# Kernel tuning notes

Hardware: AMD Instinct MI355X
Metric: run time of the kernel (lower is better)

## Reference

```python
import jax, jax.numpy as jnp
import numpy as np

B, C, H, W = 16, 64, 64, 64
HEADS = 8

def conv1x1(x, w):
    # x: [B, Cin, H, W], w: [Cout, Cin] -> [B, Cout, H, W]
    return jnp.einsum('oc,bchw->bohw', w, x)

def maxpool2x2(x):
    b, c, h, w = x.shape
    return x.reshape(b, c, h // 2, 2, w // 2, 2).max(axis=(3, 5))

def setup_inputs() -> dict:
    key = jax.random.key(0)
    ks = jax.random.split(key, 6)
    x = jax.random.normal(ks[0], (B, C, H, W), dtype=jnp.float32)
    w_theta = jax.random.normal(ks[1], (C // HEADS, C), dtype=jnp.float32) * 0.05
    w_phi = jax.random.normal(ks[2], (C // HEADS, C), dtype=jnp.float32) * 0.05
    w_g = jax.random.normal(ks[3], (C // 2, C), dtype=jnp.float32) * 0.05
    w_o = jax.random.normal(ks[4], (C, C // 2), dtype=jnp.float32) * 0.05
    gamma = jax.random.normal(ks[5], (), dtype=jnp.float32)
    return {'x': x, 'w_theta': w_theta, 'w_phi': w_phi, 'w_g': w_g, 'w_o': w_o, 'gamma': gamma}

def reference(x, w_theta, w_phi, w_g, w_o, gamma):
    b, c, h, w = x.shape
    n = h * w                      # query length
    m = n // 4                     # kv length after 2x2 maxpool
    theta = conv1x1(x, w_theta).reshape(b, c // HEADS, n)   # [B, C/h, N]
    phi = maxpool2x2(conv1x1(x, w_phi)).reshape(b, c // HEADS, m)  # [B, C/h, M]
    g = maxpool2x2(conv1x1(x, w_g)).reshape(b, c // 2, m)   # [B, C/2, M]
    # attention: theta^T @ phi -> [B, N, M]; NOTE: no 1/sqrt(d) scaling (SAGAN)
    beta = jax.nn.softmax(jnp.einsum('bdn,bdm->bnm', theta, phi), axis=-1)
    # o = g @ beta^T -> [B, C/2, N]
    o = jnp.einsum('bdm,bnm->bdn', g, beta).reshape(b, c // 2, h, w)
    o = conv1x1(o, w_o)            # [B, C, H, W]
    return gamma * o + x
```

## Files before the change

kernel.cpp:

```cpp
#include <hip/hip_runtime.h>
#include <hip/hip_bf16.h>

#define NB 16
#define NC 64
#define NN 4096
#define NM 1024
#define ND 8
#define NG 32

typedef short short8 __attribute__((ext_vector_type(8)));
typedef float floatx4 __attribute__((ext_vector_type(4)));

#define LOG2E 1.44269504f

__device__ __forceinline__ short f2bfs(float f) {
    union { __hip_bfloat16 h; short s; } u;
    u.h = __float2bfloat16(f);
    return u.s;
}
__device__ __forceinline__ unsigned pack2bf(float a, float b) {
    return (unsigned)(unsigned short)f2bfs(a) | ((unsigned)(unsigned short)f2bfs(b) << 16);
}
__device__ __forceinline__ unsigned pk2fast(float a, float b) {
    unsigned ua = __float_as_uint(a) + 0x8000u;
    unsigned ub = __float_as_uint(b) + 0x8000u;
    return __builtin_amdgcn_perm(ub, ua, 0x07060302);
}
__device__ __forceinline__ short8 u4s8(uint4 v) {
    union { uint4 u; short8 s; } c; c.u = v; return c.s;
}

__global__ __launch_bounds__(256)
void proj_kernel(const float* __restrict__ x,
                 const float* __restrict__ w_phi,
                 const float* __restrict__ w_g,
                 const float* __restrict__ w_o,
                 unsigned* __restrict__ phi_ws,
                 unsigned* __restrict__ g2_ws)
{
    __shared__ __align__(16) float xl[64 * 128];
    __shared__ float lwpT[64 * 8];
    __shared__ __align__(8) float lwgT[64 * 34];
    __shared__ float lwoT[32 * 65];
    __shared__ __align__(16) float lgs[32 * 36];
    __shared__ float lps[32 * 8];

    const int b  = blockIdx.x >> 5;
    const int ph = blockIdx.x & 31;
    const int t  = threadIdx.x;

    for (int i = t; i < 512; i += 256) lwpT[(i & 63) * 8 + (i >> 6)] = w_phi[i];
    for (int i = t; i < 2048; i += 256) {
        lwgT[(i & 63) * 34 + (i >> 6)] = w_g[i];
        lwoT[(i & 31) * 65 + (i >> 5)] = w_o[i];
    }

    const float* xb = x + (size_t)b * NC * NN + (size_t)ph * 128;
    for (int idx = t; idx < 2048; idx += 256) {
        int c = idx >> 5, i4 = idx & 31;
        ((float4*)xl)[c * 32 + i4] = ((const float4*)(xb + (size_t)c * NN))[i4];
    }
    __syncthreads();

    {
        int oc = t >> 3, grp = t & 7;
        float s0[16];
        #pragma unroll
        for (int i = 0; i < 16; ++i) s0[i] = 0.f;
        const float4* xl4 = (const float4*)xl;
        #pragma unroll 4
        for (int c = 0; c < 64; ++c) {
            float4 a0 = xl4[c * 32 + 2 * grp];
            float4 a1 = xl4[c * 32 + 2 * grp + 1];
            float4 b0 = xl4[c * 32 + 16 + 2 * grp];
            float4 b1 = xl4[c * 32 + 17 + 2 * grp];
            float w0 = lwgT[c * 34 + oc];
            s0[0] = fmaf(w0, a0.x, s0[0]);  s0[1] = fmaf(w0, a0.y, s0[1]);
            s0[2] = fmaf(w0, a0.z, s0[2]);  s0[3] = fmaf(w0, a0.w, s0[3]);
            s0[4] = fmaf(w0, a1.x, s0[4]);  s0[5] = fmaf(w0, a1.y, s0[5]);
            s0[6] = fmaf(w0, a1.z, s0[6]);  s0[7] = fmaf(w0, a1.w, s0[7]);
            s0[8] = fmaf(w0, b0.x, s0[8]);  s0[9] = fmaf(w0, b0.y, s0[9]);
            s0[10] = fmaf(w0, b0.z, s0[10]); s0[11] = fmaf(w0, b0.w, s0[11]);
            s0[12] = fmaf(w0, b1.x, s0[12]); s0[13] = fmaf(w0, b1.y, s0[13]);
            s0[14] = fmaf(w0, b1.z, s0[14]); s0[15] = fmaf(w0, b1.w, s0[15]);
        }
        #pragma unroll
        for (int p = 0; p < 4; ++p)
            lgs[oc * 36 + grp * 4 + p] =
                fmaxf(fmaxf(s0[2 * p], s0[2 * p + 1]), fmaxf(s0[8 + 2 * p], s0[9 + 2 * p]));
    }

    {
        int m = t >> 3, oc = t & 7;
        float s0 = 0.f, s1 = 0.f, s2 = 0.f, s3 = 0.f;
        #pragma unroll 4
        for (int c = 0; c < 64; ++c) {
            float w = lwpT[c * 8 + oc];
            const float* xr = &xl[c * 128];
            s0 = fmaf(w, xr[2 * m],      s0);
            s1 = fmaf(w, xr[2 * m + 1],  s1);
            s2 = fmaf(w, xr[64 + 2 * m], s2);
            s3 = fmaf(w, xr[65 + 2 * m], s3);
        }
        lps[m * 8 + oc] = fmaxf(fmaxf(s0, s1), fmaxf(s2, s3));
    }
    __syncthreads();

    {
        int co = t >> 2, sel = t & 3;
        int m0a = 4 * sel, m0b = 16 + 4 * sel;
        float v[8];
        #pragma unroll
        for (int mm = 0; mm < 8; ++mm) v[mm] = 0.f;
        #pragma unroll 4
        for (int c = 0; c < 32; ++c) {
            float w = lwoT[c * 65 + co];
            float4 ga = *(const float4*)&lgs[c * 36 + m0a];
            float4 gb = *(const float4*)&lgs[c * 36 + m0b];
            v[0] = fmaf(w, ga.x, v[0]); v[1] = fmaf(w, ga.y, v[1]);
            v[2] = fmaf(w, ga.z, v[2]); v[3] = fmaf(w, ga.w, v[3]);
            v[4] = fmaf(w, gb.x, v[4]); v[5] = fmaf(w, gb.y, v[5]);
            v[6] = fmaf(w, gb.z, v[6]); v[7] = fmaf(w, gb.w, v[7]);
        }
        uint4 pk;
        pk.x = pack2bf(v[0], v[1]); pk.y = pack2bf(v[2], v[3]);
        pk.z = pack2bf(v[4], v[5]); pk.w = pack2bf(v[6], v[7]);
        int lane = (sel << 4) | (co & 15);
        ((uint4*)g2_ws)[(((size_t)b * 4 + (co >> 4)) * 32 + ph) * 64 + lane] = pk;
    }

    if (t < 32) {
        const float* pr = &lps[t * 8];
        uint4 pk;
        pk.x = pack2bf(pr[0], pr[1]); pk.y = pack2bf(pr[2], pr[3]);
        pk.z = pack2bf(pr[4], pr[5]); pk.w = pack2bf(pr[6], pr[7]);
        ((uint4*)phi_ws)[(size_t)b * NM + ph * 32 + t] = pk;
    }
}

#define KG_STEP(CPP0, CPP1, CG)                                                          \
    {                                                                                    \
        _Pragma("unroll")                                                                \
        for (int qt = 0; qt < 2; ++qt) {                                                 \
            floatx4 s0 = __builtin_amdgcn_mfma_f32_16x16x32_bf16(                        \
                u4s8(CPP0), u4s8(tb[qt]), (floatx4)0.f, 0, 0, 0);                        \
            floatx4 s1 = __builtin_amdgcn_mfma_f32_16x16x32_bf16(                        \
                u4s8(CPP1), u4s8(tb[qt]), (floatx4)0.f, 0, 0, 0);                        \
            float e0[4], e1[4];                                                          \
            _Pragma("unroll")                                                            \
            for (int r = 0; r < 4; ++r) {                                                \
                e0[r] = __builtin_amdgcn_exp2f(s0[r]);                                   \
                e1[r] = __builtin_amdgcn_exp2f(s1[r]);                                   \
            }                                                                            \
            lsum[qt] += ((e0[0] + e0[1]) + (e0[2] + e0[3]))                              \
                      + ((e1[0] + e1[1]) + (e1[2] + e1[3]));                             \
            uint4 pb = make_uint4(pk2fast(e0[0], e0[1]), pk2fast(e0[2], e0[3]),          \
                                  pk2fast(e1[0], e1[1]), pk2fast(e1[2], e1[3]));         \
            _Pragma("unroll")                                                            \
            for (int ct = 0; ct < 4; ++ct)                                               \
                acc[qt][ct] = __builtin_amdgcn_mfma_f32_16x16x32_bf16(                   \
                    u4s8(CG[ct]), u4s8(pb), acc[qt][ct], 0, 0, 0);                       \
        }                                                                                \
    }

__global__ __launch_bounds__(256, 2)
void attn_kernel(const unsigned* __restrict__ phi_ws,
                 const unsigned* __restrict__ g2_ws,
                 const float* __restrict__ w_theta,
                 const float* __restrict__ gamma_p,
                 const float* __restrict__ x,
                 float* __restrict__ out)
{
    __shared__ __align__(16) float smem[14080];
    uint4* lphi = (uint4*)smem;
    float* lwt  = smem + 4096;
    float* lth  = smem + 4608;
    float* lx   = smem + 5632;
    float* ltr  = smem + 4608;

    const int b    = blockIdx.x >> 5;
    const int qblk = blockIdx.x & 31;
    const int t    = threadIdx.x;
    const int w    = t >> 6;
    const int lane = t & 63;
    const int lm   = lane & 15;
    const int quad = lane >> 4;
    const int q0   = qblk * 128 + w * 32;

    const uint4* gf = (const uint4*)g2_ws;
    uint4 gA[4], gB[4];
    #pragma unroll
    for (int ct = 0; ct < 4; ++ct) {
        gA[ct] = gf[(((size_t)b * 4 + ct) * 32 + 0) * 64 + lane];
        gB[ct] = gf[(((size_t)b * 4 + ct) * 32 + 1) * 64 + lane];
    }

    for (int kk = t; kk < NM; kk += 256)
        lphi[kk] = ((const uint4*)phi_ws)[(size_t)b * NM + kk];
    for (int i = t; i < 512; i += 256) lwt[i] = w_theta[i];
    {
        const float* xb = x + (size_t)b * NC * NN + (size_t)qblk * 128;
        for (int idx = t; idx < 2048; idx += 256) {
            int c = idx >> 5, i4 = idx & 31;
            ((float4*)(lx + c * 132))[i4] = ((const float4*)(xb + (size_t)c * NN))[i4];
        }
    }
    __syncthreads();

    {
        int qi = t & 127, och = (t >> 7) * 4;
        float th4[4] = {0.f, 0.f, 0.f, 0.f};
        for (int c = 0; c < 64; ++c) {
            float xv = lx[c * 132 + qi];
            #pragma unroll
            for (int o = 0; o < 4; ++o)
                th4[o] = fmaf(lwt[(och + o) * 64 + c], xv, th4[o]);
        }
        *(float4*)&lth[qi * 8 + och] = make_float4(th4[0], th4[1], th4[2], th4[3]);
    }
    __syncthreads();

    uint4 tb[2];
    #pragma unroll
    for (int qt = 0; qt < 2; ++qt) {
        const float* thp = &lth[(w * 32 + qt * 16 + lm) * 8];
        float4 a = ((const float4*)thp)[0], c4 = ((const float4*)thp)[1];
        uint4 v;
        v.x = pack2bf(a.x * LOG2E, a.y * LOG2E);
        v.y = pack2bf(a.z * LOG2E, a.w * LOG2E);
        v.z = pack2bf(c4.x * LOG2E, c4.y * LOG2E);
        v.w = pack2bf(c4.z * LOG2E, c4.w * LOG2E);
        tb[qt].x = quad == 0 ? v.x : 0u;
        tb[qt].y = quad == 0 ? v.y : 0u;
        tb[qt].z = quad == 0 ? v.z : 0u;
        tb[qt].w = quad == 0 ? v.w : 0u;
    }

    floatx4 acc[2][4];
    #pragma unroll
    for (int qt = 0; qt < 2; ++qt)
        #pragma unroll
        for (int ct = 0; ct < 4; ++ct) acc[qt][ct] = (floatx4)0.f;
    float lsum[2] = {0.f, 0.f};

    uint4 qA0 = lphi[lm],      qA1 = lphi[16 + lm];
    uint4 qB0 = lphi[32 + lm], qB1 = lphi[48 + lm];

    for (int kg2 = 0; kg2 < 16; ++kg2) {
        {
            uint4 c0 = qA0, c1 = qA1;
            uint4 cg[4] = {gA[0], gA[1], gA[2], gA[3]};
            if (kg2 < 15) {
                int nk = 2 * kg2 + 2;
                qA0 = lphi[nk * 32 + lm];
                qA1 = lphi[nk * 32 + 16 + lm];
                #pragma unroll
                for (int ct = 0; ct < 4; ++ct)
                    gA[ct] = gf[(((size_t)b * 4 + ct) * 32 + nk) * 64 + lane];
            }
            KG_STEP(c0, c1, cg);
        }
        {
            uint4 c0 = qB0, c1 = qB1;
            uint4 cg[4] = {gB[0], gB[1], gB[2], gB[3]};
            if (kg2 < 15) {
                int nk = 2 * kg2 + 3;
                qB0 = lphi[nk * 32 + lm];
                qB1 = lphi[nk * 32 + 16 + lm];
                #pragma unroll
                for (int ct = 0; ct < 4; ++ct)
                    gB[ct] = gf[(((size_t)b * 4 + ct) * 32 + nk) * 64 + lane];
            }
            KG_STEP(c0, c1, cg);
        }
    }

    float inv[2];
    {
        float l0 = lsum[0]; l0 += __shfl_xor(l0, 16); l0 += __shfl_xor(l0, 32);
        float l1 = lsum[1]; l1 += __shfl_xor(l1, 16); l1 += __shfl_xor(l1, 32);
        inv[0] = 1.0f / l0; inv[1] = 1.0f / l1;
    }

    const float gamma = gamma_p[0];

    __syncthreads();
    #pragma unroll
    for (int qt = 0; qt < 2; ++qt)
        #pragma unroll
        for (int ct = 0; ct < 4; ++ct)
            #pragma unroll
            for (int r = 0; r < 4; ++r)
                ltr[(ct * 16 + quad * 4 + r) * 140 + w * 32 + qt * 16 + lm]
                    = acc[qt][ct][r] * inv[qt];
    __syncthreads();

    {
        const int l16 = t & 15;
        #pragma unroll
        for (int io = 0; io < 4; ++io) {
            int co = io * 16 + (t >> 4);
            size_t base = ((size_t)b * NC + co) * NN + qblk * 128 + l16 * 8;
            const float* tr = &ltr[co * 140 + l16 * 8];
            float4 t0 = ((const float4*)tr)[0];
            float4 t1 = ((const float4*)tr)[1];
            float4 x0 = *(const float4*)(x + base);
            float4 x1 = *(const float4*)(x + base + 4);
            float4 o0 = make_float4(fmaf(gamma, t0.x, x0.x), fmaf(gamma, t0.y, x0.y),
                                    fmaf(gamma, t0.z, x0.z), fmaf(gamma, t0.w, x0.w));
            float4 o1 = make_float4(fmaf(gamma, t1.x, x1.x), fmaf(gamma, t1.y, x1.y),
                                    fmaf(gamma, t1.z, x1.z), fmaf(gamma, t1.w, x1.w));
            *(float4*)(out + base)     = o0;
            *(float4*)(out + base + 4) = o1;
        }
    }
}

extern "C" void kernel_launch(void* const* d_in, const int* in_sizes, int n_in,
                              void* d_out, int out_size, void* d_ws, size_t ws_size,
                              hipStream_t stream)
{
    const float* x  = (const float*)d_in[0];
    const float* wt = (const float*)d_in[1];
    const float* wp = (const float*)d_in[2];
    const float* wg = (const float*)d_in[3];
    const float* wo = (const float*)d_in[4];
    const float* gm = (const float*)d_in[5];
    float* out = (float*)d_out;

    unsigned* phi_ws = (unsigned*)d_ws;
    unsigned* g2_ws  = phi_ws + (size_t)NB * NM * ND / 2;

    proj_kernel<<<NB * 32, 256, 0, stream>>>(x, wp, wg, wo, phi_ws, g2_ws);
    attn_kernel<<<NB * 32, 256, 0, stream>>>(phi_ws, g2_ws, wt, gm, x, out);
}
```

Before: 113.8 us.

## Fuse projection and attention kernels with per-batch atomic flag barrier

Merges the projection kernel and the attention kernel into a single launch. Each block computes its slice of phi and the w_o-folded g, publishes it to workspace, then spins on a per-batch atomic counter until all 32 blocks of that batch are done before loading the full phi and g. The x tile is loaded once and kept in registers for the residual add, so the second global read of x goes away. The cost is a memset launch and a software grid barrier that assumes all 512 blocks can be co-resident; otherwise it deadlocks. Blocks also spin-wait on their slowest sibling.

New measurement: 210.2 us. 84.7% more time.

```diff
diff --git a/kernel.cpp b/kernel.cpp
--- a/kernel.cpp
+++ b/kernel.cpp
@@ -30,115 +30,7 @@
     union { uint4 u; short8 s; } c; c.u = v; return c.s;
 }
 
-__global__ __launch_bounds__(256)
-void proj_kernel(const float* __restrict__ x,
-                 const float* __restrict__ w_phi,
-                 const float* __restrict__ w_g,
-                 const float* __restrict__ w_o,
-                 unsigned* __restrict__ phi_ws,
-                 unsigned* __restrict__ g2_ws)
-{
-    __shared__ __align__(16) float xl[64 * 128];
-    __shared__ float lwpT[64 * 8];
-    __shared__ __align__(8) float lwgT[64 * 34];
-    __shared__ float lwoT[32 * 65];
-    __shared__ __align__(16) float lgs[32 * 36];
-    __shared__ float lps[32 * 8];
-
-    const int b  = blockIdx.x >> 5;
-    const int ph = blockIdx.x & 31;
-    const int t  = threadIdx.x;
-
-    for (int i = t; i < 512; i += 256) lwpT[(i & 63) * 8 + (i >> 6)] = w_phi[i];
-    for (int i = t; i < 2048; i += 256) {
-        lwgT[(i & 63) * 34 + (i >> 6)] = w_g[i];
-        lwoT[(i & 31) * 65 + (i >> 5)] = w_o[i];
-    }
-
-    const float* xb = x + (size_t)b * NC * NN + (size_t)ph * 128;
-    for (int idx = t; idx < 2048; idx += 256) {
-        int c = idx >> 5, i4 = idx & 31;
-        ((float4*)xl)[c * 32 + i4] = ((const float4*)(xb + (size_t)c * NN))[i4];
-    }
-    __syncthreads();
-
-    {
-        int oc = t >> 3, grp = t & 7;
-        float s0[16];
-        #pragma unroll
-        for (int i = 0; i < 16; ++i) s0[i] = 0.f;
-        const float4* xl4 = (const float4*)xl;
-        #pragma unroll 4
-        for (int c = 0; c < 64; ++c) {
-            float4 a0 = xl4[c * 32 + 2 * grp];
-            float4 a1 = xl4[c * 32 + 2 * grp + 1];
-            float4 b0 = xl4[c * 32 + 16 + 2 * grp];
-            float4 b1 = xl4[c * 32 + 17 + 2 * grp];
-            float w0 = lwgT[c * 34 + oc];
-            s0[0] = fmaf(w0, a0.x, s0[0]);  s0[1] = fmaf(w0, a0.y, s0[1]);
-            s0[2] = fmaf(w0, a0.z, s0[2]);  s0[3] = fmaf(w0, a0.w, s0[3]);
-            s0[4] = fmaf(w0, a1.x, s0[4]);  s0[5] = fmaf(w0, a1.y, s0[5]);
-            s0[6] = fmaf(w0, a1.z, s0[6]);  s0[7] = fmaf(w0, a1.w, s0[7]);
-            s0[8] = fmaf(w0, b0.x, s0[8]);  s0[9] = fmaf(w0, b0.y, s0[9]);
-            s0[10] = fmaf(w0, b0.z, s0[10]); s0[11] = fmaf(w0, b0.w, s0[11]);
-            s0[12] = fmaf(w0, b1.x, s0[12]); s0[13] = fmaf(w0, b1.y, s0[13]);
-            s0[14] = fmaf(w0, b1.z, s0[14]); s0[15] = fmaf(w0, b1.w, s0[15]);
-        }
-        #pragma unroll
-        for (int p = 0; p < 4; ++p)
-            lgs[oc * 36 + grp * 4 + p] =
-                fmaxf(fmaxf(s0[2 * p], s0[2 * p + 1]), fmaxf(s0[8 + 2 * p], s0[9 + 2 * p]));
-    }
-
-    {
-        int m = t >> 3, oc = t & 7;
-        float s0 = 0.f, s1 = 0.f, s2 = 0.f, s3 = 0.f;
-        #pragma unroll 4
-        for (int c = 0; c < 64; ++c) {
-            float w = lwpT[c * 8 + oc];
-            const float* xr = &xl[c * 128];
-            s0 = fmaf(w, xr[2 * m],      s0);
-            s1 = fmaf(w, xr[2 * m + 1],  s1);
-            s2 = fmaf(w, xr[64 + 2 * m], s2);
-            s3 = fmaf(w, xr[65 + 2 * m], s3);
-        }
-        lps[m * 8 + oc] = fmaxf(fmaxf(s0, s1), fmaxf(s2, s3));
-    }
-    __syncthreads();
-
-    {
-        int co = t >> 2, sel = t & 3;
-        int m0a = 4 * sel, m0b = 16 + 4 * sel;
-        float v[8];
-        #pragma unroll
-        for (int mm = 0; mm < 8; ++mm) v[mm] = 0.f;
-        #pragma unroll 4
-        for (int c = 0; c < 32; ++c) {
-            float w = lwoT[c * 65 + co];
-            float4 ga = *(const float4*)&lgs[c * 36 + m0a];
-            float4 gb = *(const float4*)&lgs[c * 36 + m0b];
-            v[0] = fmaf(w, ga.x, v[0]); v[1] = fmaf(w, ga.y, v[1]);
-            v[2] = fmaf(w, ga.z, v[2]); v[3] = fmaf(w, ga.w, v[3]);
-            v[4] = fmaf(w, gb.x, v[4]); v[5] = fmaf(w, gb.y, v[5]);
-            v[6] = fmaf(w, gb.z, v[6]); v[7] = fmaf(w, gb.w, v[7]);
-        }
-        uint4 pk;
-        pk.x = pack2bf(v[0], v[1]); pk.y = pack2bf(v[2], v[3]);
-        pk.z = pack2bf(v[4], v[5]); pk.w = pack2bf(v[6], v[7]);
-        int lane = (sel << 4) | (co & 15);
-        ((uint4*)g2_ws)[(((size_t)b * 4 + (co >> 4)) * 32 + ph) * 64 + lane] = pk;
-    }
-
-    if (t < 32) {
-        const float* pr = &lps[t * 8];
-        uint4 pk;
-        pk.x = pack2bf(pr[0], pr[1]); pk.y = pack2bf(pr[2], pr[3]);
-        pk.z = pack2bf(pr[4], pr[5]); pk.w = pack2bf(pr[6], pr[7]);
-        ((uint4*)phi_ws)[(size_t)b * NM + ph * 32 + t] = pk;
-    }
-}
-
-#define KG_STEP(CPP0, CPP1, CG)                                                          \
+#define KG_STEP(CPP0, CPP1, CG_)                                                         \
     {                                                                                    \
         _Pragma("unroll")                                                                \
         for (int qt = 0; qt < 2; ++qt) {                                                 \
@@ -159,53 +51,111 @@
             _Pragma("unroll")                                                            \
             for (int ct = 0; ct < 4; ++ct)                                               \
                 acc[qt][ct] = __builtin_amdgcn_mfma_f32_16x16x32_bf16(                   \
-                    u4s8(CG[ct]), u4s8(pb), acc[qt][ct], 0, 0, 0);                       \
+                    u4s8(CG_[ct]), u4s8(pb), acc[qt][ct], 0, 0, 0);                      \
         }                                                                                \
     }
 
 __global__ __launch_bounds__(256, 2)
-void attn_kernel(const unsigned* __restrict__ phi_ws,
-                 const unsigned* __restrict__ g2_ws,
-                 const float* __restrict__ w_theta,
-                 const float* __restrict__ gamma_p,
-                 const float* __restrict__ x,
-                 float* __restrict__ out)
+void fused_kernel(const float* __restrict__ x,
+                  const float* __restrict__ w_theta,
+                  const float* __restrict__ w_phi,
+                  const float* __restrict__ w_g,
+                  const float* __restrict__ w_o,
+                  const float* __restrict__ gamma_p,
+                  unsigned* __restrict__ phi_ws,
+                  unsigned* __restrict__ g2_ws,
+                  int* __restrict__ flags,
+                  float* __restrict__ out)
 {
-    __shared__ __align__(16) float smem[14080];
-    uint4* lphi = (uint4*)smem;
-    float* lwt  = smem + 4096;
-    float* lth  = smem + 4608;
-    float* lx   = smem + 5632;
-    float* ltr  = smem + 4608;
+    __shared__ __align__(16) float smem[16096];
+    float* lx   = smem;
+    float* lwpT = smem + 8448;
+    float* lwgT = smem + 8960;
+    float* lwoT = smem + 11072;
+    float* lgs  = smem + 13152;
+    float* lps  = smem + 14304;
+    float* lwt  = smem + 14560;
+    float* lth  = smem + 15072;
+    uint4* lphi = (uint4*)(smem + 8960);
+    float* ltr  = smem;
 
     const int b    = blockIdx.x >> 5;
-    const int qblk = blockIdx.x & 31;
+    const int ph   = blockIdx.x & 31;
     const int t    = threadIdx.x;
     const int w    = t >> 6;
     const int lane = t & 63;
     const int lm   = lane & 15;
     const int quad = lane >> 4;
-    const int q0   = qblk * 128 + w * 32;
-
-    const uint4* gf = (const uint4*)g2_ws;
-    uint4 gA[4], gB[4];
-    #pragma unroll
-    for (int ct = 0; ct < 4; ++ct) {
-        gA[ct] = gf[(((size_t)b * 4 + ct) * 32 + 0) * 64 + lane];
-        gB[ct] = gf[(((size_t)b * 4 + ct) * 32 + 1) * 64 + lane];
-    }
-
-    for (int kk = t; kk < NM; kk += 256)
-        lphi[kk] = ((const uint4*)phi_ws)[(size_t)b * NM + kk];
-    for (int i = t; i < 512; i += 256) lwt[i] = w_theta[i];
-    {
-        const float* xb = x + (size_t)b * NC * NN + (size_t)qblk * 128;
-        for (int idx = t; idx < 2048; idx += 256) {
-            int c = idx >> 5, i4 = idx & 31;
-            ((float4*)(lx + c * 132))[i4] = ((const float4*)(xb + (size_t)c * NN))[i4];
-        }
-    }
-    __syncthreads();
+
+    for (int i = t; i < 512; i += 256) {
+        lwpT[(i & 63) * 8 + (i >> 6)] = w_phi[i];
+        lwt[i] = w_theta[i];
+    }
+    for (int i = t; i < 2048; i += 256) {
+        lwgT[(i & 63) * 33 + (i >> 6)] = w_g[i];
+        lwoT[(i & 31) * 65 + (i >> 5)] = w_o[i];
+    }
+    const float* xb = x + (size_t)b * NC * NN + (size_t)ph * 128;
+    for (int idx = t; idx < 2048; idx += 256) {
+        int c = idx >> 5, i4 = idx & 31;
+        ((float4*)(lx + c * 132))[i4] = ((const float4*)(xb + (size_t)c * NN))[i4];
+    }
+    __syncthreads();
+
+    float4 xr0[4], xr1[4];
+    {
+        const int l16 = t & 15;
+        #pragma unroll
+        for (int io = 0; io < 4; ++io) {
+            int co = io * 16 + (t >> 4);
+            const float* p = &lx[co * 132 + l16 * 8];
+            xr0[io] = ((const float4*)p)[0];
+            xr1[io] = ((const float4*)p)[1];
+        }
+    }
+
+    {
+        int oc = t >> 3, grp = t & 7;
+        float s0[16];
+        #pragma unroll
+        for (int i = 0; i < 16; ++i) s0[i] = 0.f;
+        const float4* xl4 = (const float4*)lx;
+        #pragma unroll 4
+        for (int c = 0; c < 64; ++c) {
+            float4 a0 = xl4[c * 33 + 2 * grp];
+            float4 a1 = xl4[c * 33 + 2 * grp + 1];
+            float4 b0 = xl4[c * 33 + 16 + 2 * grp];
+            float4 b1 = xl4[c * 33 + 17 + 2 * grp];
+            float w0 = lwgT[c * 33 + oc];
+            s0[0] = fmaf(w0, a0.x, s0[0]);  s0[1] = fmaf(w0, a0.y, s0[1]);
+            s0[2] = fmaf(w0, a0.z, s0[2]);  s0[3] = fmaf(w0, a0.w, s0[3]);
+            s0[4] = fmaf(w0, a1.x, s0[4]);  s0[5] = fmaf(w0, a1.y, s0[5]);
+            s0[6] = fmaf(w0, a1.z, s0[6]);  s0[7] = fmaf(w0, a1.w, s0[7]);
+            s0[8] = fmaf(w0, b0.x, s0[8]);  s0[9] = fmaf(w0, b0.y, s0[9]);
+            s0[10] = fmaf(w0, b0.z, s0[10]); s0[11] = fmaf(w0, b0.w, s0[11]);
+            s0[12] = fmaf(w0, b1.x, s0[12]); s0[13] = fmaf(w0, b1.y, s0[13]);
+            s0[14] = fmaf(w0, b1.z, s0[14]); s0[15] = fmaf(w0, b1.w, s0[15]);
+        }
+        #pragma unroll
+        for (int p = 0; p < 4; ++p)
+            lgs[oc * 36 + grp * 4 + p] =
+                fmaxf(fmaxf(s0[2 * p], s0[2 * p + 1]), fmaxf(s0[8 + 2 * p], s0[9 + 2 * p]));
+    }
+
+    {
+        int m = t >> 3, oc = t & 7;
+        float s0 = 0.f, s1 = 0.f, s2 = 0.f, s3 = 0.f;
+        #pragma unroll 4
+        for (int c = 0; c < 64; ++c) {
+            float wv = lwpT[c * 8 + oc];
+            const float* xr = &lx[c * 132];
+            s0 = fmaf(wv, xr[2 * m],      s0);
+            s1 = fmaf(wv, xr[2 * m + 1],  s1);
+            s2 = fmaf(wv, xr[64 + 2 * m], s2);
+            s3 = fmaf(wv, xr[65 + 2 * m], s3);
+        }
+        lps[m * 8 + oc] = fmaxf(fmaxf(s0, s1), fmaxf(s2, s3));
+    }
 
     {
         int qi = t & 127, och = (t >> 7) * 4;
@@ -219,6 +169,37 @@
         *(float4*)&lth[qi * 8 + och] = make_float4(th4[0], th4[1], th4[2], th4[3]);
     }
     __syncthreads();
+
+    {
+        int co = t >> 2, sel = t & 3;
+        int m0a = 4 * sel, m0b = 16 + 4 * sel;
+        float v[8];
+        #pragma unroll
+        for (int mm = 0; mm < 8; ++mm) v[mm] = 0.f;
+        #pragma unroll 4
+        for (int c = 0; c < 32; ++c) {
+            float wv = lwoT[c * 65 + co];
+            float4 ga = *(const float4*)&lgs[c * 36 + m0a];
+            float4 gb = *(const float4*)&lgs[c * 36 + m0b];
+            v[0] = fmaf(wv, ga.x, v[0]); v[1] = fmaf(wv, ga.y, v[1]);
+            v[2] = fmaf(wv, ga.z, v[2]); v[3] = fmaf(wv, ga.w, v[3]);
+            v[4] = fmaf(wv, gb.x, v[4]); v[5] = fmaf(wv, gb.y, v[5]);
+            v[6] = fmaf(wv, gb.z, v[6]); v[7] = fmaf(wv, gb.w, v[7]);
+        }
+        uint4 pk;
+        pk.x = pack2bf(v[0], v[1]); pk.y = pack2bf(v[2], v[3]);
+        pk.z = pack2bf(v[4], v[5]); pk.w = pack2bf(v[6], v[7]);
+        int ln = (sel << 4) | (co & 15);
+        ((uint4*)g2_ws)[(((size_t)b * 4 + (co >> 4)) * 32 + ph) * 64 + ln] = pk;
+    }
+
+    if (t < 32) {
+        const float* pr = &lps[t * 8];
+        uint4 pk;
+        pk.x = pack2bf(pr[0], pr[1]); pk.y = pack2bf(pr[2], pr[3]);
+        pk.z = pack2bf(pr[4], pr[5]); pk.w = pack2bf(pr[6], pr[7]);
+        ((uint4*)phi_ws)[(size_t)b * NM + ph * 32 + t] = pk;
+    }
 
     uint4 tb[2];
     #pragma unroll
@@ -236,6 +217,29 @@
         tb[qt].w = quad == 0 ? v.w : 0u;
     }
 
+    __threadfence();
+    __syncthreads();
+    if (t == 0) {
+        __hip_atomic_fetch_add(&flags[b], 1, __ATOMIC_RELEASE,
+                               __HIP_MEMORY_SCOPE_AGENT);
+        while (__hip_atomic_load(&flags[b], __ATOMIC_ACQUIRE,
+                                 __HIP_MEMORY_SCOPE_AGENT) < 32)
+            __builtin_amdgcn_s_sleep(2);
+    }
+    __syncthreads();
+    __threadfence();
+
+    const uint4* gf = (const uint4*)g2_ws;
+    uint4 gA[4], gB[4];
+    #pragma unroll
+    for (int ct = 0; ct < 4; ++ct) {
+        gA[ct] = gf[(((size_t)b * 4 + ct) * 32 + 0) * 64 + lane];
+        gB[ct] = gf[(((size_t)b * 4 + ct) * 32 + 1) * 64 + lane];
+    }
+    for (int kk = t; kk < NM; kk += 256)
+        lphi[kk] = ((const uint4*)phi_ws)[(size_t)b * NM + kk];
+    __syncthreads();
+
     floatx4 acc[2][4];
     #pragma unroll
     for (int qt = 0; qt < 2; ++qt)
@@ -300,16 +304,14 @@
         #pragma unroll
         for (int io = 0; io < 4; ++io) {
             int co = io * 16 + (t >> 4);
-            size_t base = ((size_t)b * NC + co) * NN + qblk * 128 + l16 * 8;
+            size_t base = ((size_t)b * NC + co) * NN + (size_t)ph * 128 + l16 * 8;
             const float* tr = &ltr[co * 140 + l16 * 8];
             float4 t0 = ((const float4*)tr)[0];
             float4 t1 = ((const float4*)tr)[1];
-            float4 x0 = *(const float4*)(x + base);
-            float4 x1 = *(const float4*)(x + base + 4);
-            float4 o0 = make_float4(fmaf(gamma, t0.x, x0.x), fmaf(gamma, t0.y, x0.y),
-                                    fmaf(gamma, t0.z, x0.z), fmaf(gamma, t0.w, x0.w));
-            float4 o1 = make_float4(fmaf(gamma, t1.x, x1.x), fmaf(gamma, t1.y, x1.y),
-                                    fmaf(gamma, t1.z, x1.z), fmaf(gamma, t1.w, x1.w));
+            float4 o0 = make_float4(fmaf(gamma, t0.x, xr0[io].x), fmaf(gamma, t0.y, xr0[io].y),
+                                    fmaf(gamma, t0.z, xr0[io].z), fmaf(gamma, t0.w, xr0[io].w));
+            float4 o1 = make_float4(fmaf(gamma, t1.x, xr1[io].x), fmaf(gamma, t1.y, xr1[io].y),
+                                    fmaf(gamma, t1.z, xr1[io].z), fmaf(gamma, t1.w, xr1[io].w));
             *(float4*)(out + base)     = o0;
             *(float4*)(out + base + 4) = o1;
         }
@@ -330,7 +332,9 @@
 
     unsigned* phi_ws = (unsigned*)d_ws;
     unsigned* g2_ws  = phi_ws + (size_t)NB * NM * ND / 2;
-
-    proj_kernel<<<NB * 32, 256, 0, stream>>>(x, wp, wg, wo, phi_ws, g2_ws);
-    attn_kernel<<<NB * 32, 256, 0, stream>>>(phi_ws, g2_ws, wt, gm, x, out);
-}
+    int* flags = (int*)((char*)d_ws + (size_t)(256 * 1024 + 2 * 1024 * 1024));
+
+    hipMemsetAsync(flags, 0, NB * sizeof(int), stream);
+    fused_kernel<<<NB * 32, 256, 0, stream>>>(x, wt, wp, wg, wo, gm,
+                                              phi_ws, g2_ws, flags, out);
+}
```
